# Kernel optimization log

Measured on AMD Instinct MI355X. Metric: run time of the kernel, lower is better.

## Reference

```python
import jax, jax.numpy as jnp
import numpy as np
import math

N = 50000      # nodes
E = 800000     # edges
F_IN = 64      # input node features
H = 4          # heads
C = 32         # hidden_channels (per-head dim)
HC = H * C     # 128
ED = 4         # edge_dim
G = 1000       # graphs in batch


def _lin(key, fin, fout, bias=True):
    k1, k2 = jax.random.split(key)
    w = jax.random.normal(k1, (fin, fout), jnp.float32) * (1.0 / math.sqrt(fin))
    if bias:
        b = jax.random.normal(k2, (fout,), jnp.float32) * 0.02
        return w, b
    return w


def setup_inputs() -> dict:
    key = jax.random.key(0)
    ks = jax.random.split(key, 24)
    x = jax.random.normal(ks[0], (N, F_IN), jnp.float32)
    edge_index = jax.random.randint(ks[1], (2, E), 0, N)
    edge_attr = jax.random.normal(ks[2], (E, ED), jnp.float32)
    batch = jnp.sort(jax.random.randint(ks[3], (N,), 0, G))
    inp = {"x": x, "edge_index": edge_index, "edge_attr": edge_attr, "batch": batch}
    fins = [F_IN, HC, HC]
    i = 4
    for l in range(3):
        fin = fins[l]
        inp[f"wq{l+1}"], inp[f"bq{l+1}"] = _lin(ks[i], fin, HC); i += 1
        inp[f"wk{l+1}"], inp[f"bk{l+1}"] = _lin(ks[i], fin, HC); i += 1
        inp[f"wv{l+1}"], inp[f"bv{l+1}"] = _lin(ks[i], fin, HC); i += 1
        inp[f"we{l+1}"] = _lin(ks[i], ED, HC, bias=False); i += 1
        inp[f"ws{l+1}"], inp[f"bs{l+1}"] = _lin(ks[i], fin, HC); i += 1
    inp["wlin"], inp["blin"] = _lin(ks[i], HC, 1)
    return inp


def _segment_softmax(alpha, seg, n):
    # numerically-stable softmax over edges grouped by destination node
    m = jax.ops.segment_max(alpha, seg, num_segments=n)
    m = jnp.where(jnp.isfinite(m), m, 0.0)
    a = jnp.exp(alpha - m[seg])
    s = jax.ops.segment_sum(a, seg, num_segments=n)
    return a / (s[seg] + 1e-16)


def _conv(x, src, dst, ea, wq, bq, wk, bk, wv, bv, we, ws, bs):
    # PyG TransformerConv (concat=True, root_weight=True, beta=False)
    n = x.shape[0]
    q = (x @ wq + bq).reshape(n, H, C)
    k = (x @ wk + bk).reshape(n, H, C)
    v = (x @ wv + bv).reshape(n, H, C)
    e = (ea @ we).reshape(-1, H, C)          # [E,H,C] edge projection
    kj = k[src] + e                           # key of source + edge
    alpha = jnp.einsum('ehc,ehc->eh', q[dst], kj) / math.sqrt(C)  # [E,H]
    alpha = _segment_softmax(alpha, dst, n)
    msg = (v[src] + e) * alpha[..., None]     # [E,H,C]
    out = jax.ops.segment_sum(msg, dst, num_segments=n).reshape(n, HC)
    return out + x @ ws + bs                  # skip connection


def reference(x, edge_index, edge_attr, batch,
              wq1, bq1, wk1, bk1, wv1, bv1, we1, ws1, bs1,
              wq2, bq2, wk2, bk2, wv2, bv2, we2, ws2, bs2,
              wq3, bq3, wk3, bk3, wv3, bv3, we3, ws3, bs3,
              wlin, blin):
    src, dst = edge_index[0], edge_index[1]
    h = jax.nn.relu(_conv(x, src, dst, edge_attr, wq1, bq1, wk1, bk1, wv1, bv1, we1, ws1, bs1))
    h = jax.nn.relu(_conv(h, src, dst, edge_attr, wq2, bq2, wk2, bk2, wv2, bv2, we2, ws2, bs2))
    h = _conv(h, src, dst, edge_attr, wq3, bq3, wk3, bk3, wv3, bv3, we3, ws3, bs3)
    # global_mean_pool
    s = jax.ops.segment_sum(h, batch, num_segments=G)
    cnt = jax.ops.segment_sum(jnp.ones((h.shape[0],), h.dtype), batch, num_segments=G)
    pooled = s / jnp.maximum(cnt, 1.0)[:, None]
    # dropout is identity in eval mode
    return pooled @ wlin + blin
```

## Files before the change

### kernel.cpp

```cpp
#include <hip/hip_runtime.h>
#include <math.h>

#define NN 50000
#define EE 800000
#define GG 1000

typedef __attribute__((ext_vector_type(4))) _Float16 h4f;
typedef __attribute__((ext_vector_type(8))) _Float16 h8f;
typedef __attribute__((ext_vector_type(4))) float f32x4;

static inline int ceil_div(int a, int b) { return (a + b - 1) / b; }

union EU { int2 i; h4f h; };


__global__ __launch_bounds__(256) void hist_k(const int* __restrict__ ei, int* __restrict__ cnt)
{
    int e = blockIdx.x * 256 + threadIdx.x;
    if (e >= EE) return;
    atomicAdd(&cnt[ei[EE + e]], 1);
}

__global__ __launch_bounds__(1024) void scan1_k(const int* __restrict__ cnt, int n,
                                                int* __restrict__ rowptr, int* __restrict__ bsum)
{
    __shared__ int tmp[1024];
    const int tid = threadIdx.x;
    const int i = blockIdx.x * 1024 + tid;
    tmp[tid] = (i < n) ? cnt[i] : 0;
    __syncthreads();
    for (int off = 1; off < 1024; off <<= 1) {
        int t = (tid >= off) ? tmp[tid - off] : 0;
        __syncthreads();
        tmp[tid] += t;
        __syncthreads();
    }
    if (i < n) rowptr[i + 1] = tmp[tid];
    if (tid == 1023) bsum[blockIdx.x] = tmp[1023];
}

__global__ __launch_bounds__(64) void scan2_k(int* __restrict__ bsum, int nb)
{
    const int t = threadIdx.x;
    int v = (t < nb) ? bsum[t] : 0;
    const int orig = v;
    for (int off = 1; off < 64; off <<= 1) {
        int n = __shfl_up(v, off);
        if (t >= off) v += n;
    }
    if (t < nb) bsum[t] = v - orig;
}

__global__ __launch_bounds__(1024) void scan3_k(int* __restrict__ rowptr,
                                                int* __restrict__ wcur,
                                                const int* __restrict__ bsum, int n)
{
    int i = blockIdx.x * 1024 + threadIdx.x;
    if (i < n) {
        int v = rowptr[i + 1] + bsum[blockIdx.x];
        rowptr[i + 1] = v;
        if (i + 1 < n) wcur[i + 1] = v;
    }
    if (i == 0) { rowptr[0] = 0; wcur[0] = 0; }
}

__global__ __launch_bounds__(256) void scatter_k(const int* __restrict__ ei,
                                                 const float4* __restrict__ ea,
                                                 int* __restrict__ wcur,
                                                 int4* __restrict__ edges)
{
    int e = blockIdx.x * 256 + threadIdx.x;
    if (e >= EE) return;
    int dst = ei[EE + e];
    int pos = atomicAdd(&wcur[dst], 1);
    float4 a = ea[e];
    EU u; u.h = h4f{(_Float16)a.x, (_Float16)a.y, (_Float16)a.z, (_Float16)a.w};
    edges[pos] = make_int4(ei[e], u.i.x, u.i.y, 0);
}

struct W12 { const float* w[12]; };

__global__ __launch_bounds__(64) void shuffle_w12(W12 ws, _Float16* __restrict__ out)
{
    const int m = blockIdx.y;
    const int K = (m < 4) ? 64 : 128;
    const int nblk = (K / 16) * 8;
    if (blockIdx.x >= nblk) return;
    const int s = blockIdx.x >> 3, c16 = blockIdx.x & 7;
    const int lane = threadIdx.x;
    const float* __restrict__ w = ws.w[m];
    const int kbase = s * 16 + (lane >> 4) * 4;
    const int col = c16 * 16 + (lane & 15);
    h4f h;
#pragma unroll
    for (int j = 0; j < 4; ++j) h[j] = (_Float16)w[(size_t)(kbase + j) * 128 + col];
    size_t base = (m < 4) ? (size_t)m * 64 * 128
                          : (size_t)4 * 64 * 128 + (size_t)(m - 4) * 128 * 128;
    reinterpret_cast<h4f*>(out + base)[(size_t)blockIdx.x * 64 + lane] = h;
}

template<int K, bool F32IN>
__global__ __launch_bounds__(256) void gemm_mfma(
    const void* __restrict__ xin, const _Float16* __restrict__ wshuf,
    const float* __restrict__ bq, const float* __restrict__ bk,
    const float* __restrict__ bv, const float* __restrict__ bs,
    _Float16* __restrict__ qout, _Float16* __restrict__ kout,
    _Float16* __restrict__ vout, float* __restrict__ skout)
{
    constexpr int KS = K / 16;
    constexpr int PADK = K + 8;
    __shared__ _Float16 xs[64 * PADK];
    __shared__ _Float16 wt[K * 128];
    const int t = threadIdx.x;
    const int bn = blockIdx.x * 64;
    if (F32IN) {
        const float* xf = (const float*)xin;
        constexpr int C4 = K / 4;
        for (int idx = t; idx < 64 * C4; idx += 256) {
            const int row = idx / C4, c4 = idx % C4;
            float4 val = make_float4(0.f, 0.f, 0.f, 0.f);
            if (bn + row < NN)
                val = reinterpret_cast<const float4*>(xf)[(size_t)(bn + row) * C4 + c4];
            h4f h = {(_Float16)val.x, (_Float16)val.y, (_Float16)val.z, (_Float16)val.w};
            *reinterpret_cast<h4f*>(&xs[row * PADK + c4 * 4]) = h;
        }
    } else {
        const _Float16* xh = (const _Float16*)xin;
        constexpr int CH = K / 8;
        for (int idx = t; idx < 64 * CH; idx += 256) {
            const int row = idx / CH, ch = idx % CH;
            h8f val = {0, 0, 0, 0, 0, 0, 0, 0};
            if (bn + row < NN)
                val = reinterpret_cast<const h8f*>(xh + (size_t)(bn + row) * K)[ch];
            *reinterpret_cast<h8f*>(&xs[row * PADK + ch * 8]) = val;
        }
    }
    __syncthreads();

    const int wid = t >> 6, lane = t & 63;
    const int rloc = wid * 16 + (lane & 15);
    const int ko = (lane >> 4) * 4;
    h4f b[KS];
#pragma unroll
    for (int s = 0; s < KS; ++s)
        b[s] = *reinterpret_cast<const h4f*>(&xs[rloc * PADK + s * 16 + ko]);

    const int node = bn + rloc;
    const int hcq = (lane >> 4) * 4;
    const float* bias[4] = {bq, bk, bv, bs};
    constexpr int WH4 = K * 128 / 4;

#pragma unroll
    for (int m = 0; m < 4; ++m) {
        const h4f* __restrict__ wg = reinterpret_cast<const h4f*>(wshuf + (size_t)m * K * 128);
        h4f* __restrict__ wl = reinterpret_cast<h4f*>(wt);
        for (int idx = t; idx < WH4; idx += 256) wl[idx] = wg[idx];
        __syncthreads();

        f32x4 acc[8];
#pragma unroll
        for (int c = 0; c < 8; ++c) acc[c] = {0, 0, 0, 0};
#pragma unroll
        for (int c = 0; c < 8; ++c)
#pragma unroll
            for (int s = 0; s < KS; ++s) {
                h4f af = wl[(s * 8 + c) * 64 + lane];
                acc[c] = __builtin_amdgcn_mfma_f32_16x16x16f16(af, b[s], acc[c], 0, 0, 0);
            }
        if (node < NN) {
            const float* bm = bias[m];
#pragma unroll
            for (int c = 0; c < 8; ++c) {
                const int hc = c * 16 + hcq;
                const float4 bb = *reinterpret_cast<const float4*>(&bm[hc]);
                float o0 = acc[c][0] + bb.x, o1 = acc[c][1] + bb.y;
                float o2 = acc[c][2] + bb.z, o3 = acc[c][3] + bb.w;
                if (m == 3) {
                    *reinterpret_cast<float4*>(&skout[(size_t)node * 128 + hc]) =
                        make_float4(o0, o1, o2, o3);
                } else {
                    _Float16* dst = (m == 0) ? qout : (m == 1) ? kout : vout;
                    h4f oh = {(_Float16)o0, (_Float16)o1, (_Float16)o2, (_Float16)o3};
                    *reinterpret_cast<h4f*>(&dst[(size_t)node * 128 + hc]) = oh;
                }
            }
        }
        __syncthreads();
    }
}

__global__ __launch_bounds__(256) void node_agg(
    const int* __restrict__ rowptr, const int4* __restrict__ edges,
    const _Float16* __restrict__ qh, const _Float16* __restrict__ kh,
    const _Float16* __restrict__ vh, const float* __restrict__ we,
    const float* __restrict__ sk, _Float16* __restrict__ houth, int relu)
{
    __shared__ float4 we_s[128];
    const int t = threadIdx.x;
    if (t < 128) we_s[t] = reinterpret_cast<const float4*>(we)[t];
    __syncthreads();
    const int node = blockIdx.x * 8 + (t >> 5);
    if (node >= NN) return;
    const int lane = t & 31;
    const int beg = rowptr[node], end = rowptr[node + 1];

    const float4 w0 = we_s[lane], w1 = we_s[32 + lane], w2 = we_s[64 + lane], w3 = we_s[96 + lane];

    const h4f qv = *reinterpret_cast<const h4f*>(&qh[(size_t)node * 128 + lane * 4]);
    const float sc = 0.17677669529663687f * 1.4426950408889634f;
    const float4 qf = make_float4((float)qv[0] * sc, (float)qv[1] * sc,
                                  (float)qv[2] * sc, (float)qv[3] * sc);

    float p0 = w0.x * qf.x + w0.y * qf.y + w0.z * qf.z + w0.w * qf.w;
    float p1 = w1.x * qf.x + w1.y * qf.y + w1.z * qf.z + w1.w * qf.w;
    float p2 = w2.x * qf.x + w2.y * qf.y + w2.z * qf.z + w2.w * qf.w;
    float p3 = w3.x * qf.x + w3.y * qf.y + w3.z * qf.z + w3.w * qf.w;
#pragma unroll
    for (int off = 1; off < 8; off <<= 1) {
        p0 += __shfl_xor(p0, off); p1 += __shfl_xor(p1, off);
        p2 += __shfl_xor(p2, off); p3 += __shfl_xor(p3, off);
    }
    const float qe0 = p0, qe1 = p1, qe2 = p2, qe3 = p3;

    float m = -INFINITY, s = 0.f;
    float4 acc = make_float4(0.f, 0.f, 0.f, 0.f);
    float T0 = 0.f, T1 = 0.f, T2 = 0.f, T3 = 0.f;

    int p = beg;
    for (; p + 3 < end; p += 4) {
        const int4 rA = edges[p], rB = edges[p + 1], rC = edges[p + 2], rD = edges[p + 3];
        EU uA, uB, uC, uD;
        uA.i = make_int2(rA.y, rA.z); uB.i = make_int2(rB.y, rB.z);
        uC.i = make_int2(rC.y, rC.z); uD.i = make_int2(rD.y, rD.z);
        const h4f kA = *reinterpret_cast<const h4f*>(&kh[(size_t)rA.x * 128 + lane * 4]);
        const h4f kB = *reinterpret_cast<const h4f*>(&kh[(size_t)rB.x * 128 + lane * 4]);
        const h4f kC = *reinterpret_cast<const h4f*>(&kh[(size_t)rC.x * 128 + lane * 4]);
        const h4f kD = *reinterpret_cast<const h4f*>(&kh[(size_t)rD.x * 128 + lane * 4]);
        const h4f vA = *reinterpret_cast<const h4f*>(&vh[(size_t)rA.x * 128 + lane * 4]);
        const h4f vB = *reinterpret_cast<const h4f*>(&vh[(size_t)rB.x * 128 + lane * 4]);
        const h4f vC = *reinterpret_cast<const h4f*>(&vh[(size_t)rC.x * 128 + lane * 4]);
        const h4f vD = *reinterpret_cast<const h4f*>(&vh[(size_t)rD.x * 128 + lane * 4]);
        float alA = qf.x * (float)kA[0] + qf.y * (float)kA[1]
                  + qf.z * (float)kA[2] + qf.w * (float)kA[3];
        float alB = qf.x * (float)kB[0] + qf.y * (float)kB[1]
                  + qf.z * (float)kB[2] + qf.w * (float)kB[3];
        float alC = qf.x * (float)kC[0] + qf.y * (float)kC[1]
                  + qf.z * (float)kC[2] + qf.w * (float)kC[3];
        float alD = qf.x * (float)kD[0] + qf.y * (float)kD[1]
                  + qf.z * (float)kD[2] + qf.w * (float)kD[3];
        alA += __shfl_xor(alA, 1); alA += __shfl_xor(alA, 2); alA += __shfl_xor(alA, 4);
        alB += __shfl_xor(alB, 1); alB += __shfl_xor(alB, 2); alB += __shfl_xor(alB, 4);
        alC += __shfl_xor(alC, 1); alC += __shfl_xor(alC, 2); alC += __shfl_xor(alC, 4);
        alD += __shfl_xor(alD, 1); alD += __shfl_xor(alD, 2); alD += __shfl_xor(alD, 4);
        const float fA0 = (float)uA.h[0], fA1 = (float)uA.h[1],
                    fA2 = (float)uA.h[2], fA3 = (float)uA.h[3];
        const float fB0 = (float)uB.h[0], fB1 = (float)uB.h[1],
                    fB2 = (float)uB.h[2], fB3 = (float)uB.h[3];
        const float fC0 = (float)uC.h[0], fC1 = (float)uC.h[1],
                    fC2 = (float)uC.h[2], fC3 = (float)uC.h[3];
        const float fD0 = (float)uD.h[0], fD1 = (float)uD.h[1],
                    fD2 = (float)uD.h[2], fD3 = (float)uD.h[3];
        alA += fA0 * qe0 + fA1 * qe1 + fA2 * qe2 + fA3 * qe3;
        alB += fB0 * qe0 + fB1 * qe1 + fB2 * qe2 + fB3 * qe3;
        alC += fC0 * qe0 + fC1 * qe1 + fC2 * qe2 + fC3 * qe3;
        alD += fD0 * qe0 + fD1 * qe1 + fD2 * qe2 + fD3 * qe3;
        const float mn = fmaxf(fmaxf(fmaxf(alA, alB), fmaxf(alC, alD)), m);
        const float r  = exp2f(m - mn);
        const float pA = exp2f(alA - mn), pB = exp2f(alB - mn);
        const float pC = exp2f(alC - mn), pD = exp2f(alD - mn);
        s = s * r + pA + pB + pC + pD;
        acc.x = acc.x * r + pA * (float)vA[0] + pB * (float)vB[0]
                          + pC * (float)vC[0] + pD * (float)vD[0];
        acc.y = acc.y * r + pA * (float)vA[1] + pB * (float)vB[1]
                          + pC * (float)vC[1] + pD * (float)vD[1];
        acc.z = acc.z * r + pA * (float)vA[2] + pB * (float)vB[2]
                          + pC * (float)vC[2] + pD * (float)vD[2];
        acc.w = acc.w * r + pA * (float)vA[3] + pB * (float)vB[3]
                          + pC * (float)vC[3] + pD * (float)vD[3];
        T0 = T0 * r + pA * fA0 + pB * fB0 + pC * fC0 + pD * fD0;
        T1 = T1 * r + pA * fA1 + pB * fB1 + pC * fC1 + pD * fD1;
        T2 = T2 * r + pA * fA2 + pB * fB2 + pC * fC2 + pD * fD2;
        T3 = T3 * r + pA * fA3 + pB * fB3 + pC * fC3 + pD * fD3;
        m = mn;
    }
    for (; p < end; ++p) {
        const int4 rA = edges[p];
        EU uA; uA.i = make_int2(rA.y, rA.z);
        const h4f kA = *reinterpret_cast<const h4f*>(&kh[(size_t)rA.x * 128 + lane * 4]);
        const h4f vA = *reinterpret_cast<const h4f*>(&vh[(size_t)rA.x * 128 + lane * 4]);
        float alA = qf.x * (float)kA[0] + qf.y * (float)kA[1]
                  + qf.z * (float)kA[2] + qf.w * (float)kA[3];
        alA += __shfl_xor(alA, 1); alA += __shfl_xor(alA, 2); alA += __shfl_xor(alA, 4);
        const float fA0 = (float)uA.h[0], fA1 = (float)uA.h[1],
                    fA2 = (float)uA.h[2], fA3 = (float)uA.h[3];
        alA += fA0 * qe0 + fA1 * qe1 + fA2 * qe2 + fA3 * qe3;
        const float mn = fmaxf(m, alA);
        const float r  = exp2f(m - mn);
        const float pA = exp2f(alA - mn);
        s = s * r + pA;
        acc.x = acc.x * r + pA * (float)vA[0];
        acc.y = acc.y * r + pA * (float)vA[1];
        acc.z = acc.z * r + pA * (float)vA[2];
        acc.w = acc.w * r + pA * (float)vA[3];
        T0 = T0 * r + pA * fA0;
        T1 = T1 * r + pA * fA1;
        T2 = T2 * r + pA * fA2;
        T3 = T3 * r + pA * fA3;
        m = mn;
    }
    const float inv = 1.0f / (s + 1e-16f);
    const float4 sk4 = *reinterpret_cast<const float4*>(&sk[(size_t)node * 128 + lane * 4]);
    float o0 = (acc.x + w0.x * T0 + w1.x * T1 + w2.x * T2 + w3.x * T3) * inv + sk4.x;
    float o1 = (acc.y + w0.y * T0 + w1.y * T1 + w2.y * T2 + w3.y * T3) * inv + sk4.y;
    float o2 = (acc.z + w0.z * T0 + w1.z * T1 + w2.z * T2 + w3.z * T3) * inv + sk4.z;
    float o3 = (acc.w + w0.w * T0 + w1.w * T1 + w2.w * T2 + w3.w * T3) * inv + sk4.w;
    if (relu) {
        o0 = fmaxf(o0, 0.f); o1 = fmaxf(o1, 0.f);
        o2 = fmaxf(o2, 0.f); o3 = fmaxf(o3, 0.f);
    }
    h4f oh = {(_Float16)o0, (_Float16)o1, (_Float16)o2, (_Float16)o3};
    *reinterpret_cast<h4f*>(&houth[(size_t)node * 128 + lane * 4]) = oh;
}


__global__ __launch_bounds__(256) void boundaries_k(const int* __restrict__ batch,
                                                    int* __restrict__ gptr)
{
    int i = blockIdx.x * 256 + threadIdx.x;
    if (i >= NN) return;
    int b = batch[i];
    int bp = (i == 0) ? -1 : batch[i - 1];
    for (int g = bp + 1; g <= b; ++g) gptr[g] = i;
    if (i == NN - 1) for (int g = b + 1; g <= GG; ++g) gptr[g] = NN;
}

__global__ __launch_bounds__(128) void head_k(
    const _Float16* __restrict__ h, const int* __restrict__ gptr,
    const float* __restrict__ wlin, const float* __restrict__ blin,
    float* __restrict__ out)
{
    __shared__ float red[128];
    const int g = blockIdx.x;
    const int t = threadIdx.x;
    const int beg = gptr[g], end = gptr[g + 1];
    float p = 0.f;
    for (int n = beg; n < end; ++n) p += (float)h[(size_t)n * 128 + t];
    p *= wlin[t];
    red[t] = p;
    __syncthreads();
    for (int off = 64; off; off >>= 1) {
        if (t < off) red[t] += red[t + off];
        __syncthreads();
    }
    if (t == 0) out[g] = red[0] / fmaxf((float)(end - beg), 1.0f) + blin[0];
}

extern "C" void kernel_launch(void* const* d_in, const int* in_sizes, int n_in,
                              void* d_out, int out_size, void* d_ws, size_t ws_size,
                              hipStream_t stream)
{
    const float* x     = (const float*)d_in[0];
    const int*   ei    = (const int*)d_in[1];
    const float* ea    = (const float*)d_in[2];
    const int*   batch = (const int*)d_in[3];
    auto W = [&](int i) { return (const float*)d_in[i]; };

    char* wsb = (char*)d_ws;
    size_t off = 0;
    auto alloc = [&](size_t bytes) { void* p = wsb + off; off += (bytes + 15) & ~15ull; return p; };

    float* sk       = (float*)alloc((size_t)NN * 128 * 4);
    int4*  edges    = (int4*)alloc((size_t)EE * 16);
    _Float16* qh    = (_Float16*)alloc((size_t)NN * 128 * 2);
    _Float16* kh    = (_Float16*)alloc((size_t)NN * 128 * 2);
    _Float16* vh    = (_Float16*)alloc((size_t)NN * 128 * 2);
    _Float16* hh    = (_Float16*)alloc((size_t)NN * 128 * 2);
    _Float16* wshuf = (_Float16*)alloc(((size_t)4 * 64 * 128 + 8 * 128 * 128) * 2);
    int* cnt    = (int*)alloc((size_t)NN * 4);
    int* rowptr = (int*)alloc((size_t)(NN + 1) * 4);
    int* wcur   = (int*)alloc((size_t)NN * 4);
    int* gptr   = (int*)alloc((size_t)(GG + 1) * 4);
    int* bsum   = (int*)alloc((size_t)64 * 4);

    hipMemsetAsync(cnt, 0, NN * sizeof(int), stream);
    hist_k<<<ceil_div(EE, 256), 256, 0, stream>>>(ei, cnt);
    const int NB = ceil_div(NN, 1024);
    scan1_k<<<NB, 1024, 0, stream>>>(cnt, NN, rowptr, bsum);
    scan2_k<<<1, 64, 0, stream>>>(bsum, NB);
    scan3_k<<<NB, 1024, 0, stream>>>(rowptr, wcur, bsum, NN);
    scatter_k<<<ceil_div(EE, 256), 256, 0, stream>>>(ei, (const float4*)ea, wcur, edges);

    boundaries_k<<<ceil_div(NN, 256), 256, 0, stream>>>(batch, gptr);

    W12 w12 = {{ W(4), W(6), W(8), W(11),
                 W(13), W(15), W(17), W(20),
                 W(22), W(24), W(26), W(29) }};
    shuffle_w12<<<dim3(64, 12), 64, 0, stream>>>(w12, wshuf);
    const size_t wsz1 = (size_t)4 * 64 * 128;
    const size_t wsz2 = (size_t)4 * 128 * 128;

    auto layer = [&](int K, const void* xin, const _Float16* wsh, int relu, int wb) {
        if (K == 64)
            gemm_mfma<64, true><<<ceil_div(NN, 64), 256, 0, stream>>>(
                xin, wsh, W(wb + 1), W(wb + 3), W(wb + 5), W(wb + 8), qh, kh, vh, sk);
        else
            gemm_mfma<128, false><<<ceil_div(NN, 64), 256, 0, stream>>>(
                xin, wsh, W(wb + 1), W(wb + 3), W(wb + 5), W(wb + 8), qh, kh, vh, sk);
        node_agg<<<ceil_div(NN, 8), 256, 0, stream>>>(
            rowptr, edges, qh, kh, vh, W(wb + 6), sk, hh, relu);
    };

    layer(64,  x,  wshuf, 1, 4);
    layer(128, hh, wshuf + wsz1, 1, 13);
    layer(128, hh, wshuf + wsz1 + wsz2, 0, 22);

    head_k<<<GG, 128, 0, stream>>>(hh, gptr, W(31), W(32), (float*)d_out);
}
```

Before: 495.0 us.

## Split node edge list across four lane groups with online-softmax merge

```diff
diff --git a/kernel.cpp b/kernel.cpp
--- a/kernel.cpp
+++ b/kernel.cpp
@@ -189,137 +189,108 @@
     }
 }
 
-__global__ __launch_bounds__(256) void node_agg(
+__global__ __launch_bounds__(256, 8) void node_agg(
     const int* __restrict__ rowptr, const int4* __restrict__ edges,
     const _Float16* __restrict__ qh, const _Float16* __restrict__ kh,
     const _Float16* __restrict__ vh, const float* __restrict__ we,
     const float* __restrict__ sk, _Float16* __restrict__ houth, int relu)
 {
-    __shared__ float4 we_s[128];
+    __shared__ float we_s[4 * 128];
     const int t = threadIdx.x;
-    if (t < 128) we_s[t] = reinterpret_cast<const float4*>(we)[t];
+    if (t < 128)
+        reinterpret_cast<float4*>(we_s)[t] = reinterpret_cast<const float4*>(we)[t];
     __syncthreads();
-    const int node = blockIdx.x * 8 + (t >> 5);
+    const int node = blockIdx.x * 4 + (t >> 6);
     if (node >= NN) return;
-    const int lane = t & 31;
+    const int lane = t & 63;
+    const int g = lane >> 4, sub = lane & 15, ch0 = sub * 8;
     const int beg = rowptr[node], end = rowptr[node + 1];
-
-    const float4 w0 = we_s[lane], w1 = we_s[32 + lane], w2 = we_s[64 + lane], w3 = we_s[96 + lane];
-
-    const h4f qv = *reinterpret_cast<const h4f*>(&qh[(size_t)node * 128 + lane * 4]);
+    const int deg = end - beg;
+
     const float sc = 0.17677669529663687f * 1.4426950408889634f;
-    const float4 qf = make_float4((float)qv[0] * sc, (float)qv[1] * sc,
-                                  (float)qv[2] * sc, (float)qv[3] * sc);
-
-    float p0 = w0.x * qf.x + w0.y * qf.y + w0.z * qf.z + w0.w * qf.w;
-    float p1 = w1.x * qf.x + w1.y * qf.y + w1.z * qf.z + w1.w * qf.w;
-    float p2 = w2.x * qf.x + w2.y * qf.y + w2.z * qf.z + w2.w * qf.w;
-    float p3 = w3.x * qf.x + w3.y * qf.y + w3.z * qf.z + w3.w * qf.w;
-#pragma unroll
-    for (int off = 1; off < 8; off <<= 1) {
-        p0 += __shfl_xor(p0, off); p1 += __shfl_xor(p1, off);
-        p2 += __shfl_xor(p2, off); p3 += __shfl_xor(p3, off);
-    }
-    const float qe0 = p0, qe1 = p1, qe2 = p2, qe3 = p3;
-
-    float m = -INFINITY, s = 0.f;
-    float4 acc = make_float4(0.f, 0.f, 0.f, 0.f);
-    float T0 = 0.f, T1 = 0.f, T2 = 0.f, T3 = 0.f;
-
-    int p = beg;
-    for (; p + 3 < end; p += 4) {
-        const int4 rA = edges[p], rB = edges[p + 1], rC = edges[p + 2], rD = edges[p + 3];
-        EU uA, uB, uC, uD;
-        uA.i = make_int2(rA.y, rA.z); uB.i = make_int2(rB.y, rB.z);
-        uC.i = make_int2(rC.y, rC.z); uD.i = make_int2(rD.y, rD.z);
-        const h4f kA = *reinterpret_cast<const h4f*>(&kh[(size_t)rA.x * 128 + lane * 4]);
-        const h4f kB = *reinterpret_cast<const h4f*>(&kh[(size_t)rB.x * 128 + lane * 4]);
-        const h4f kC = *reinterpret_cast<const h4f*>(&kh[(size_t)rC.x * 128 + lane * 4]);
-        const h4f kD = *reinterpret_cast<const h4f*>(&kh[(size_t)rD.x * 128 + lane * 4]);
-        const h4f vA = *reinterpret_cast<const h4f*>(&vh[(size_t)rA.x * 128 + lane * 4]);
-        const h4f vB = *reinterpret_cast<const h4f*>(&vh[(size_t)rB.x * 128 + lane * 4]);
-        const h4f vC = *reinterpret_cast<const h4f*>(&vh[(size_t)rC.x * 128 + lane * 4]);
-        const h4f vD = *reinterpret_cast<const h4f*>(&vh[(size_t)rD.x * 128 + lane * 4]);
-        float alA = qf.x * (float)kA[0] + qf.y * (float)kA[1]
-                  + qf.z * (float)kA[2] + qf.w * (float)kA[3];
-        float alB = qf.x * (float)kB[0] + qf.y * (float)kB[1]
-                  + qf.z * (float)kB[2] + qf.w * (float)kB[3];
-        float alC = qf.x * (float)kC[0] + qf.y * (float)kC[1]
-                  + qf.z * (float)kC[2] + qf.w * (float)kC[3];
-        float alD = qf.x * (float)kD[0] + qf.y * (float)kD[1]
-                  + qf.z * (float)kD[2] + qf.w * (float)kD[3];
-        alA += __shfl_xor(alA, 1); alA += __shfl_xor(alA, 2); alA += __shfl_xor(alA, 4);
-        alB += __shfl_xor(alB, 1); alB += __shfl_xor(alB, 2); alB += __shfl_xor(alB, 4);
-        alC += __shfl_xor(alC, 1); alC += __shfl_xor(alC, 2); alC += __shfl_xor(alC, 4);
-        alD += __shfl_xor(alD, 1); alD += __shfl_xor(alD, 2); alD += __shfl_xor(alD, 4);
-        const float fA0 = (float)uA.h[0], fA1 = (float)uA.h[1],
-                    fA2 = (float)uA.h[2], fA3 = (float)uA.h[3];
-        const float fB0 = (float)uB.h[0], fB1 = (float)uB.h[1],
-                    fB2 = (float)uB.h[2], fB3 = (float)uB.h[3];
-        const float fC0 = (float)uC.h[0], fC1 = (float)uC.h[1],
-                    fC2 = (float)uC.h[2], fC3 = (float)uC.h[3];
-        const float fD0 = (float)uD.h[0], fD1 = (float)uD.h[1],
-                    fD2 = (float)uD.h[2], fD3 = (float)uD.h[3];
-        alA += fA0 * qe0 + fA1 * qe1 + fA2 * qe2 + fA3 * qe3;
-        alB += fB0 * qe0 + fB1 * qe1 + fB2 * qe2 + fB3 * qe3;
-        alC += fC0 * qe0 + fC1 * qe1 + fC2 * qe2 + fC3 * qe3;
-        alD += fD0 * qe0 + fD1 * qe1 + fD2 * qe2 + fD3 * qe3;
-        const float mn = fmaxf(fmaxf(fmaxf(alA, alB), fmaxf(alC, alD)), m);
-        const float r  = exp2f(m - mn);
-        const float pA = exp2f(alA - mn), pB = exp2f(alB - mn);
-        const float pC = exp2f(alC - mn), pD = exp2f(alD - mn);
-        s = s * r + pA + pB + pC + pD;
-        acc.x = acc.x * r + pA * (float)vA[0] + pB * (float)vB[0]
-                          + pC * (float)vC[0] + pD * (float)vD[0];
-        acc.y = acc.y * r + pA * (float)vA[1] + pB * (float)vB[1]
-                          + pC * (float)vC[1] + pD * (float)vD[1];
-        acc.z = acc.z * r + pA * (float)vA[2] + pB * (float)vB[2]
-                          + pC * (float)vC[2] + pD * (float)vD[2];
-        acc.w = acc.w * r + pA * (float)vA[3] + pB * (float)vB[3]
-                          + pC * (float)vC[3] + pD * (float)vD[3];
-        T0 = T0 * r + pA * fA0 + pB * fB0 + pC * fC0 + pD * fD0;
-        T1 = T1 * r + pA * fA1 + pB * fB1 + pC * fC1 + pD * fD1;
-        T2 = T2 * r + pA * fA2 + pB * fB2 + pC * fC2 + pD * fD2;
-        T3 = T3 * r + pA * fA3 + pB * fB3 + pC * fC3 + pD * fD3;
+    const h8f q8 = *reinterpret_cast<const h8f*>(&qh[(size_t)node * 128 + ch0]);
+    float qf[8];
+#pragma unroll
+    for (int j = 0; j < 8; ++j) qf[j] = (float)q8[j] * sc;
+
+    float qe[4];
+#pragma unroll
+    for (int d = 0; d < 4; ++d) {
+        float pq = 0.f;
+#pragma unroll
+        for (int j = 0; j < 8; ++j) pq += we_s[d * 128 + ch0 + j] * qf[j];
+        pq += __shfl_xor(pq, 1); pq += __shfl_xor(pq, 2);
+        qe[d] = pq;
+    }
+
+    float m = -1e38f, s = 0.f;
+    float acc[8] = {0, 0, 0, 0, 0, 0, 0, 0};
+    float T[4] = {0, 0, 0, 0};
+
+    const int nt = (deg + 3) >> 2;
+    int p = beg + g;
+    for (int i = 0; i < nt; ++i, p += 4) {
+        const bool act = p < end;
+        const int pc = act ? p : beg;
+        const int4 r = edges[pc];
+        EU u; u.i = make_int2(r.y, r.z);
+        const h8f k8 = *reinterpret_cast<const h8f*>(&kh[(size_t)r.x * 128 + ch0]);
+        const h8f v8 = *reinterpret_cast<const h8f*>(&vh[(size_t)r.x * 128 + ch0]);
+        float al = 0.f;
+#pragma unroll
+        for (int j = 0; j < 8; ++j) al += qf[j] * (float)k8[j];
+        al += __shfl_xor(al, 1); al += __shfl_xor(al, 2);
+        const float f0 = (float)u.h[0], f1 = (float)u.h[1],
+                    f2 = (float)u.h[2], f3 = (float)u.h[3];
+        al += f0 * qe[0] + f1 * qe[1] + f2 * qe[2] + f3 * qe[3];
+        al = act ? al : -1e38f;
+        const float mn = fmaxf(m, al);
+        const float rr = exp2f(m - mn);
+        const float pe = exp2f(al - mn);
+        s = s * rr + pe;
+#pragma unroll
+        for (int j = 0; j < 8; ++j) acc[j] = acc[j] * rr + pe * (float)v8[j];
+        T[0] = T[0] * rr + pe * f0; T[1] = T[1] * rr + pe * f1;
+        T[2] = T[2] * rr + pe * f2; T[3] = T[3] * rr + pe * f3;
         m = mn;
     }
-    for (; p < end; ++p) {
-        const int4 rA = edges[p];
-        EU uA; uA.i = make_int2(rA.y, rA.z);
-        const h4f kA = *reinterpret_cast<const h4f*>(&kh[(size_t)rA.x * 128 + lane * 4]);
-        const h4f vA = *reinterpret_cast<const h4f*>(&vh[(size_t)rA.x * 128 + lane * 4]);
-        float alA = qf.x * (float)kA[0] + qf.y * (float)kA[1]
-                  + qf.z * (float)kA[2] + qf.w * (float)kA[3];
-        alA += __shfl_xor(alA, 1); alA += __shfl_xor(alA, 2); alA += __shfl_xor(alA, 4);
-        const float fA0 = (float)uA.h[0], fA1 = (float)uA.h[1],
-                    fA2 = (float)uA.h[2], fA3 = (float)uA.h[3];
-        alA += fA0 * qe0 + fA1 * qe1 + fA2 * qe2 + fA3 * qe3;
-        const float mn = fmaxf(m, alA);
-        const float r  = exp2f(m - mn);
-        const float pA = exp2f(alA - mn);
-        s = s * r + pA;
-        acc.x = acc.x * r + pA * (float)vA[0];
-        acc.y = acc.y * r + pA * (float)vA[1];
-        acc.z = acc.z * r + pA * (float)vA[2];
-        acc.w = acc.w * r + pA * (float)vA[3];
-        T0 = T0 * r + pA * fA0;
-        T1 = T1 * r + pA * fA1;
-        T2 = T2 * r + pA * fA2;
-        T3 = T3 * r + pA * fA3;
+
+#pragma unroll
+    for (int off = 16; off <= 32; off <<= 1) {
+        const float mo = __shfl_xor(m, off);
+        const float so = __shfl_xor(s, off);
+        const float mn = fmaxf(m, mo);
+        const float r1 = exp2f(m - mn), r2 = exp2f(mo - mn);
+        s = s * r1 + so * r2;
+#pragma unroll
+        for (int j = 0; j < 8; ++j) {
+            const float ao = __shfl_xor(acc[j], off);
+            acc[j] = acc[j] * r1 + ao * r2;
+        }
+#pragma unroll
+        for (int d = 0; d < 4; ++d) {
+            const float To = __shfl_xor(T[d], off);
+            T[d] = T[d] * r1 + To * r2;
+        }
         m = mn;
     }
-    const float inv = 1.0f / (s + 1e-16f);
-    const float4 sk4 = *reinterpret_cast<const float4*>(&sk[(size_t)node * 128 + lane * 4]);
-    float o0 = (acc.x + w0.x * T0 + w1.x * T1 + w2.x * T2 + w3.x * T3) * inv + sk4.x;
-    float o1 = (acc.y + w0.y * T0 + w1.y * T1 + w2.y * T2 + w3.y * T3) * inv + sk4.y;
-    float o2 = (acc.z + w0.z * T0 + w1.z * T1 + w2.z * T2 + w3.z * T3) * inv + sk4.z;
-    float o3 = (acc.w + w0.w * T0 + w1.w * T1 + w2.w * T2 + w3.w * T3) * inv + sk4.w;
-    if (relu) {
-        o0 = fmaxf(o0, 0.f); o1 = fmaxf(o1, 0.f);
-        o2 = fmaxf(o2, 0.f); o3 = fmaxf(o3, 0.f);
-    }
-    h4f oh = {(_Float16)o0, (_Float16)o1, (_Float16)o2, (_Float16)o3};
-    *reinterpret_cast<h4f*>(&houth[(size_t)node * 128 + lane * 4]) = oh;
+
+    if (g == 0) {
+        const float inv = 1.0f / (s + 1e-16f);
+        const float4 s0 = *reinterpret_cast<const float4*>(&sk[(size_t)node * 128 + ch0]);
+        const float4 s1 = *reinterpret_cast<const float4*>(&sk[(size_t)node * 128 + ch0 + 4]);
+        const float skv[8] = {s0.x, s0.y, s0.z, s0.w, s1.x, s1.y, s1.z, s1.w};
+        h8f oh;
+#pragma unroll
+        for (int j = 0; j < 8; ++j) {
+            const float wT = we_s[0 * 128 + ch0 + j] * T[0] + we_s[1 * 128 + ch0 + j] * T[1]
+                           + we_s[2 * 128 + ch0 + j] * T[2] + we_s[3 * 128 + ch0 + j] * T[3];
+            float ov = (acc[j] + wT) * inv + skv[j];
+            if (relu) ov = fmaxf(ov, 0.f);
+            oh[j] = (_Float16)ov;
+        }
+        *reinterpret_cast<h8f*>(&houth[(size_t)node * 128 + ch0]) = oh;
+    }
 }
 
 
@@ -406,7 +377,7 @@
         else
             gemm_mfma<128, false><<<ceil_div(NN, 64), 256, 0, stream>>>(
                 xin, wsh, W(wb + 1), W(wb + 3), W(wb + 5), W(wb + 8), qh, kh, vh, sk);
-        node_agg<<<ceil_div(NN, 8), 256, 0, stream>>>(
+        node_agg<<<ceil_div(NN, 4), 256, 0, stream>>>(
             rowptr, edges, qh, kh, vh, W(wb + 6), sk, hh, relu);
     };
 
```

Result: faster. 477.7 us (-3.5%).
